# Optimization experiments

Measured on AMD Instinct MI355X. Metric: run time of the kernel, lower is better.

Reference implementation:

```python
import jax, jax.numpy as jnp
import numpy as np

UNITS = 512
LN_EPS = 1e-3  # Keras LayerNormalization default epsilon


def _lstm_cell(x, h, c, W, U, b):
    # Keras LSTMCell: z = x@W + h@U + b, gate order [i, f, g, o]
    z = x @ W + h @ U + b
    i, f, g, o = jnp.split(z, 4, axis=-1)
    i = jax.nn.sigmoid(i)
    f = jax.nn.sigmoid(f)
    g = jnp.tanh(g)
    o = jax.nn.sigmoid(o)
    c_new = f * c + i * g
    h_new = o * jnp.tanh(c_new)
    return h_new, c_new


def _layernorm(x, gamma, beta):
    mu = jnp.mean(x, axis=-1, keepdims=True)
    var = jnp.mean(jnp.square(x - mu), axis=-1, keepdims=True)
    return (x - mu) * jax.lax.rsqrt(var + LN_EPS) * gamma + beta


def setup_inputs() -> dict:
    key = jax.random.key(0)
    ks = jax.random.split(key, 8)
    B, T, F, U, C = 128, 1000, 72, UNITS, 14
    s = 0.05
    return {
        "x": jax.random.normal(ks[0], (B, T, F), jnp.float32),
        "w0": jax.random.normal(ks[1], (F, 4 * U), jnp.float32) * s,
        "u0": jax.random.normal(ks[2], (U, 4 * U), jnp.float32) * s,
        "b0": jnp.zeros((4 * U,), jnp.float32),
        "gamma": jnp.ones((U,), jnp.float32),
        "beta": jnp.zeros((U,), jnp.float32),
        "w1": jax.random.normal(ks[3], (U, 4 * U), jnp.float32) * s,
        "u1": jax.random.normal(ks[4], (U, 4 * U), jnp.float32) * s,
        "b1": jnp.zeros((4 * U,), jnp.float32),
        "wf": jax.random.normal(ks[5], (U, C), jnp.float32) * s,
        "bf": jnp.zeros((C,), jnp.float32),
    }


def reference(x, w0, u0, b0, gamma, beta, w1, u1, b1, wf, bf):
    B = x.shape[0]
    U = UNITS
    xt = jnp.transpose(x, (1, 0, 2))  # [T, B, F] time-major
    init = (
        jnp.zeros((B, U), x.dtype), jnp.zeros((B, U), x.dtype),  # h0, c0
        jnp.zeros((B, U), x.dtype), jnp.zeros((B, U), x.dtype),  # h1, c1
    )

    def step(carry, x_t):
        h0, c0, h1, c1 = carry
        h0, c0 = _lstm_cell(x_t, h0, c0, w0, u0, b0)
        h0n = _layernorm(h0, gamma, beta)
        h1, c1 = _lstm_cell(h0n, h1, c1, w1, u1, b1)
        # dropout is identity at inference (training=False)
        y_t = jax.nn.softmax(h1 @ wf + bf, axis=-1)
        return (h0, c0, h1, c1), y_t

    _, ys = jax.lax.scan(step, init, xt)  # ys: [T, B, C]
    return jnp.transpose(ys, (1, 0, 2))   # [B, T, C]
```

## Files before the change

### kernel.cpp

```cpp
#include <hip/hip_runtime.h>
#include <cstdint>
#include <cstddef>

#define T_STEPS 1000
#define NU      512
#define NC      14
#define K0TOT   592
#define K1TOT   1024

#define OFF_BP0   0
#define SZ_BP0    (128*K0TOT*16)
#define OFF_BP1   (OFF_BP0 + SZ_BP0)
#define SZ_BP1    (128*K1TOT*16)
#define OFF_S1P   (OFF_BP1 + SZ_BP1)
#define OFF_ZB1P  (OFF_S1P + 2048)
#define OFF_B0P   (OFF_ZB1P + 2048)
#define OFF_H0T   (OFF_B0P + 2048)
#define OFF_H1T   (OFF_H0T + 2*65536)
#define OFF_H1N   (OFF_H1T + 2*65536)
#define OFF_WFT   (OFF_H1N + 2*65536)
#define OFF_BAR   (OFF_WFT + 14*512)

__global__ void pack0_kernel(const float* __restrict__ w0, const float* __restrict__ u0,
                             float* __restrict__ bp0)
{
    int blk = blockIdx.x;
    int ntile = blk / 10, kc = blk % 10;
    int k0 = kc * 64;
#pragma unroll
    for (int p = 0; p < 4; p++) {
        int e = threadIdx.x + p * 256;
        int kr = e >> 4, c = e & 15;
        int k = k0 + kr;
        if (k < K0TOT) {
            int u = c >> 2, g = c & 3;
            int zcol = ntile * 4 + u + 512 * g;
            float v;
            if (k < 72)        v = w0[k * 2048 + zcol];
            else if (k < 80)   v = 0.f;
            else               v = u0[(k - 80) * 2048 + zcol];
            bp0[((size_t)ntile * K0TOT + k) * 16 + c] = v;
        }
    }
}

__global__ void pack1_kernel(const float* __restrict__ w1, const float* __restrict__ u1,
                             const float* __restrict__ gamma, float* __restrict__ bp1)
{
    int blk = blockIdx.x;
    int ntile = blk >> 4, kc = blk & 15;
    int k0 = kc * 64;
#pragma unroll
    for (int p = 0; p < 4; p++) {
        int e = threadIdx.x + p * 256;
        int kr = e >> 4, c = e & 15;
        int k = k0 + kr;
        int u = c >> 2, g = c & 3;
        int zcol = ntile * 4 + u + 512 * g;
        float v = (k < NU) ? gamma[k] * w1[k * 2048 + zcol]
                           : u1[(k - NU) * 2048 + zcol];
        bp1[((size_t)ntile * K1TOT + k) * 16 + c] = v;
    }
}

__global__ void sums_kernel(const float* __restrict__ w1, const float* __restrict__ gamma,
                            const float* __restrict__ beta, const float* __restrict__ b0,
                            const float* __restrict__ b1,
                            float* __restrict__ s1p, float* __restrict__ zb1p,
                            float* __restrict__ b0p)
{
    int zcol = blockIdx.x * 256 + threadIdx.x;
    float gs = 0.f, bs = 0.f;
    for (int k = 0; k < NU; k++) {
        float w = w1[k * 2048 + zcol];
        gs += gamma[k] * w;
        bs += beta[k] * w;
    }
    int g = zcol >> 9, r = zcol & 511, nt = r >> 2, u = r & 3;
    int pc = nt * 16 + u * 4 + g;
    s1p[pc]  = gs;
    zb1p[pc] = b1[zcol] + bs;
    b0p[pc]  = b0[zcol];
}

__global__ void wft_kernel(const float* __restrict__ wf, float* __restrict__ wfT)
{
    int i = blockIdx.x * 512 + threadIdx.x;
    if (i < NC * NU) {
        int c = i >> 9, u = i & 511;
        wfT[c * NU + u] = wf[u * NC + c];
    }
}

__global__ void init_kernel(float* __restrict__ ws)
{
    size_t i = (size_t)blockIdx.x * 1024 + threadIdx.x;
    if (i < (size_t)6 * 65536) ws[OFF_H0T + i] = 0.f;
    if (i == 0) *((unsigned*)(ws + OFF_BAR)) = 0u;
}

__device__ __forceinline__ float sigf(float x)     { return 1.f / (1.f + __expf(-x)); }
__device__ __forceinline__ float tanhfast(float x) { return 2.f / (1.f + __expf(-2.f * x)) - 1.f; }

__device__ __forceinline__ void fma8(float acc[8], float a, float4 b0, float4 b1)
{
    acc[0] = fmaf(a, b0.x, acc[0]); acc[1] = fmaf(a, b0.y, acc[1]);
    acc[2] = fmaf(a, b0.z, acc[2]); acc[3] = fmaf(a, b0.w, acc[3]);
    acc[4] = fmaf(a, b1.x, acc[4]); acc[5] = fmaf(a, b1.y, acc[5]);
    acc[6] = fmaf(a, b1.z, acc[6]); acc[7] = fmaf(a, b1.w, acc[7]);
}

__device__ __forceinline__ void reduce_zex(float acc[4][8], float* __restrict__ zex,
                                           int kw, int ch, int rg, int ks)
{
#pragma unroll
    for (int r = 0; r < 4; ++r)
#pragma unroll
        for (int c = 0; c < 8; ++c) {
            float v = acc[r][c];
            v += __shfl_xor(v, 16);
            v += __shfl_xor(v, 32);
            acc[r][c] = v;
        }
    const int zb = kw * 1088 + ch * 8;
#pragma unroll
    for (int r = 0; r < 4; ++r) {
        if (ks == r) {
#pragma unroll
            for (int c = 0; c < 8; ++c)
                zex[zb + (rg * 4 + r) * 17 + c] = acc[r][c];
        }
    }
}

__device__ __forceinline__ void grid_barrier(unsigned* bar)
{
    __syncthreads();
    if (threadIdx.x == 0) {
        __threadfence();
        unsigned old = __hip_atomic_fetch_add(bar, 1u, __ATOMIC_RELAXED, __HIP_MEMORY_SCOPE_AGENT);
        unsigned target = (old | 255u) + 1u;
        while (__hip_atomic_load(bar, __ATOMIC_RELAXED, __HIP_MEMORY_SCOPE_AGENT) < target)
            __builtin_amdgcn_s_sleep(2);
        __threadfence();
    }
    __syncthreads();
}

__device__ void ypass(const float* __restrict__ h1r, const float* __restrict__ wfT,
                      const float* __restrict__ bf, float* __restrict__ out,
                      int b, int tw, int lane)
{
    const float* hr = h1r + (size_t)b * NU + lane * 8;
    float4 hA = *(const float4*)hr;
    float4 hB = *(const float4*)(hr + 4);
    float z[NC];
#pragma unroll
    for (int c = 0; c < NC; ++c) {
        const float* wp = wfT + c * NU + lane * 8;
        float4 wA = *(const float4*)wp;
        float4 wB = *(const float4*)(wp + 4);
        float a = hA.x * wA.x;
        a = fmaf(hA.y, wA.y, a); a = fmaf(hA.z, wA.z, a); a = fmaf(hA.w, wA.w, a);
        a = fmaf(hB.x, wB.x, a); a = fmaf(hB.y, wB.y, a);
        a = fmaf(hB.z, wB.z, a); a = fmaf(hB.w, wB.w, a);
        z[c] = a;
    }
#pragma unroll
    for (int off = 32; off > 0; off >>= 1) {
#pragma unroll
        for (int c = 0; c < NC; ++c) z[c] += __shfl_xor(z[c], off);
    }
    if (lane == 0) {
        float m = -1e30f;
#pragma unroll
        for (int c = 0; c < NC; ++c) { z[c] += bf[c]; m = fmaxf(m, z[c]); }
        float s = 0.f, e[NC];
#pragma unroll
        for (int c = 0; c < NC; ++c) { e[c] = __expf(z[c] - m); s += e[c]; }
        float inv = 1.f / s;
        float* o = out + ((size_t)b * T_STEPS + tw) * NC;
#pragma unroll
        for (int c = 0; c < NC; ++c) o[c] = e[c] * inv;
    }
}

__global__ __launch_bounds__(512, 2)
void lstm_main(const float* __restrict__ x,
               const float* __restrict__ bf,
               float* __restrict__ ws, float* __restrict__ out)
{
    __shared__ float bpA_lds[K0TOT * 16];
    __shared__ float bpB_lds[K1TOT * 16];
    __shared__ float xs[64 * 81];
    __shared__ float zex[4 * 64 * 17];
    __shared__ float sq[64 * 17];

    const float* __restrict__ bp0g = ws + OFF_BP0;
    const float* __restrict__ bp1g = ws + OFF_BP1;
    const float* __restrict__ s1p  = ws + OFF_S1P;
    const float* __restrict__ zb1p = ws + OFF_ZB1P;
    const float* __restrict__ b0p  = ws + OFF_B0P;
    float* __restrict__ h0T = ws + OFF_H0T;
    float* __restrict__ h1T = ws + OFF_H1T;
    float* __restrict__ h1n = ws + OFF_H1N;
    const float* __restrict__ wfT = ws + OFF_WFT;
    unsigned* bar = (unsigned*)(ws + OFF_BAR);

    const int tid  = threadIdx.x;
    const int lane = tid & 63;
    const int w    = tid >> 6;
    const int kw   = w >> 1;
    const int ch   = w & 1;
    const int rg   = lane & 15;
    const int ks   = lane >> 4;
    const int rg4  = rg * 4;
    const int blk = blockIdx.x;
    const int mtile = blk & 1, ntile = blk >> 1;
    const int rb = mtile * 64;

    {
        const float* s0 = bp0g + (size_t)ntile * (K0TOT * 16);
        for (int i = tid; i < K0TOT * 16; i += 512) bpA_lds[i] = s0[i];
        const float* s1 = bp1g + (size_t)ntile * (K1TOT * 16);
        for (int i = tid; i < K1TOT * 16; i += 512) bpB_lds[i] = s1[i];
        for (int i = tid; i < 64 * 81; i += 512) xs[i] = 0.f;
    }
    __syncthreads();

    const int eb = tid & 63, eu = (tid >> 6) & 3;
    float c0v = 0.f, c1v = 0.f;
    float4 b0v = {0,0,0,0}, s1v = {0,0,0,0}, zbv = {0,0,0,0};
    if (tid < 256) {
        b0v = *(const float4*)&b0p[ntile * 16 + eu * 4];
        s1v = *(const float4*)&s1p[ntile * 16 + eu * 4];
        zbv = *(const float4*)&zb1p[ntile * 16 + eu * 4];
    }
    const float* xrowbase = x + (size_t)rb * 72000;

#pragma unroll 1
    for (int t = 0; t < T_STEPS; ++t) {
        const float* __restrict__ h0prev  = h0T + ((t + 1) & 1) * 65536;
        float* __restrict__       h0cur   = h0T + (t & 1) * 65536;
        const float* __restrict__ h1prev  = h1T + ((t + 1) & 1) * 65536;
        float* __restrict__       h1cur   = h1T + (t & 1) * 65536;
        const float* __restrict__ h1nprev = h1n + ((t + 1) & 1) * 65536;
        float* __restrict__       h1ncur  = h1n + (t & 1) * 65536;

        float xr[9];
#pragma unroll
        for (int j = 0; j < 9; ++j) {
            int e = tid + j * 512, row = e / 72, f = e - row * 72;
            xr[j] = xrowbase[(size_t)row * 72000 + t * 72 + f];
        }
#pragma unroll
        for (int j = 0; j < 9; ++j) {
            int e = tid + j * 512, row = e / 72, f = e - row * 72;
            xs[row * 81 + f] = xr[j];
        }
        __syncthreads();

        {
            float acc[4][8];
#pragma unroll
            for (int r = 0; r < 4; ++r)
#pragma unroll
                for (int c = 0; c < 8; ++c) acc[r][c] = 0.f;

            if (kw == 0) {
#pragma unroll 4
                for (int i = 0; i < 20; ++i) {
                    const int k = 4 * i + ks;
                    const float* bp = &bpA_lds[k * 16 + ch * 8];
                    const float4 bA = *(const float4*)bp;
                    const float4 bB = *(const float4*)(bp + 4);
                    fma8(acc[0], xs[(rg4 + 0) * 81 + k], bA, bB);
                    fma8(acc[1], xs[(rg4 + 1) * 81 + k], bA, bB);
                    fma8(acc[2], xs[(rg4 + 2) * 81 + k], bA, bB);
                    fma8(acc[3], xs[(rg4 + 3) * 81 + k], bA, bB);
                }
#pragma unroll 4
                for (int i = 20; i < 37; ++i) {
                    const int k = 4 * i + ks;
                    const float4 av = *(const float4*)(h0prev + (size_t)(k - 80) * 128 + rb + rg4);
                    const float* bp = &bpA_lds[k * 16 + ch * 8];
                    const float4 bA = *(const float4*)bp;
                    const float4 bB = *(const float4*)(bp + 4);
                    fma8(acc[0], av.x, bA, bB); fma8(acc[1], av.y, bA, bB);
                    fma8(acc[2], av.z, bA, bB); fma8(acc[3], av.w, bA, bB);
                }
            } else {
                const int kbase = kw * 148;
#pragma unroll 4
                for (int i = 0; i < 37; ++i) {
                    const int k = kbase + 4 * i + ks;
                    const float4 av = *(const float4*)(h0prev + (size_t)(k - 80) * 128 + rb + rg4);
                    const float* bp = &bpA_lds[k * 16 + ch * 8];
                    const float4 bA = *(const float4*)bp;
                    const float4 bB = *(const float4*)(bp + 4);
                    fma8(acc[0], av.x, bA, bB); fma8(acc[1], av.y, bA, bB);
                    fma8(acc[2], av.z, bA, bB); fma8(acc[3], av.w, bA, bB);
                }
            }
            reduce_zex(acc, zex, kw, ch, rg, ks);
        }
        __syncthreads();
        if (tid < 256) {
            float z[4];
#pragma unroll
            for (int g = 0; g < 4; ++g) {
                int ci = eb * 17 + eu * 4 + g;
                z[g] = zex[ci] + zex[1088 + ci] + zex[2176 + ci] + zex[3264 + ci];
            }
            z[0] += b0v.x; z[1] += b0v.y; z[2] += b0v.z; z[3] += b0v.w;
            float ig = sigf(z[0]), fg = sigf(z[1]), gg = tanhfast(z[2]), og = sigf(z[3]);
            float cn = fg * c0v + ig * gg;
            c0v = cn;
            h0cur[(ntile * 4 + eu) * 128 + rb + eb] = og * tanhfast(cn);
        }

        grid_barrier(bar);

        {
            float s = 0.f, q = 0.f;
            const float* hp = h0cur + (size_t)(w * 64) * 128 + rb + lane;
#pragma unroll 8
            for (int kk = 0; kk < 64; ++kk) {
                float v = hp[(size_t)kk * 128];
                s += v; q = fmaf(v, v, q);
            }
            sq[lane * 17 + w * 2]     = s;
            sq[lane * 17 + w * 2 + 1] = q;
        }

        if (blk < 128 && w == 0 && t > 0) ypass(h1nprev, wfT, bf, out, blk, t - 1, lane);

        {
            float acc[4][8];
#pragma unroll
            for (int r = 0; r < 4; ++r)
#pragma unroll
                for (int c = 0; c < 8; ++c) acc[r][c] = 0.f;

            const float* __restrict__ Asrc = (kw < 2) ? h0cur : h1prev;
            const int kofs   = (kw & 1) * 256;
            const int kb_lds = kw * 256;
#pragma unroll 4
            for (int i = 0; i < 64; ++i) {
                const int kk = 4 * i + ks;
                const float4 av = *(const float4*)(Asrc + (size_t)(kofs + kk) * 128 + rb + rg4);
                const float* bp = &bpB_lds[(kb_lds + kk) * 16 + ch * 8];
                const float4 bA = *(const float4*)bp;
                const float4 bB = *(const float4*)(bp + 4);
                fma8(acc[0], av.x, bA, bB); fma8(acc[1], av.y, bA, bB);
                fma8(acc[2], av.z, bA, bB); fma8(acc[3], av.w, bA, bB);
            }
            reduce_zex(acc, zex, kw, ch, rg, ks);
        }
        __syncthreads();
        if (tid < 256) {
            float s = 0.f, q = 0.f;
#pragma unroll
            for (int w8 = 0; w8 < 8; ++w8) {
                s += sq[eb * 17 + w8 * 2];
                q += sq[eb * 17 + w8 * 2 + 1];
            }
            float m  = s * (1.f / 512.f);
            float rs = rsqrtf(q * (1.f / 512.f) - m * m + 1e-3f);
            float z[4];
#pragma unroll
            for (int g = 0; g < 4; ++g) {
                int ci = eb * 17 + eu * 4 + g;
                float zG = zex[ci] + zex[1088 + ci];
                float zU = zex[2176 + ci] + zex[3264 + ci];
                float s1g = (g == 0) ? s1v.x : (g == 1) ? s1v.y : (g == 2) ? s1v.z : s1v.w;
                float zbg = (g == 0) ? zbv.x : (g == 1) ? zbv.y : (g == 2) ? zbv.z : zbv.w;
                z[g] = rs * (zG - m * s1g) + zU + zbg;
            }
            float ig = sigf(z[0]), fg = sigf(z[1]), gg = tanhfast(z[2]), og = sigf(z[3]);
            float cn = fg * c1v + ig * gg;
            c1v = cn;
            float hv = og * tanhfast(cn);
            h1cur[(ntile * 4 + eu) * 128 + rb + eb] = hv;
            h1ncur[(size_t)(rb + eb) * 512 + ntile * 4 + eu] = hv;
        }
    }

    grid_barrier(bar);
    if (blk < 128 && w == 0)
        ypass(h1n + ((T_STEPS - 1) & 1) * 65536, wfT, bf, out, blk, T_STEPS - 1, lane);
}

extern "C" void kernel_launch(void* const* d_in, const int* in_sizes, int n_in,
                              void* d_out, int out_size, void* d_ws, size_t ws_size,
                              hipStream_t stream)
{
    const float* x     = (const float*)d_in[0];
    const float* w0    = (const float*)d_in[1];
    const float* u0    = (const float*)d_in[2];
    const float* b0    = (const float*)d_in[3];
    const float* gamma = (const float*)d_in[4];
    const float* beta  = (const float*)d_in[5];
    const float* w1    = (const float*)d_in[6];
    const float* u1    = (const float*)d_in[7];
    const float* b1    = (const float*)d_in[8];
    const float* wf    = (const float*)d_in[9];
    const float* bf    = (const float*)d_in[10];
    float* out = (float*)d_out;
    float* ws  = (float*)d_ws;

    hipLaunchKernelGGL(pack0_kernel, dim3(128 * 10), dim3(256), 0, stream, w0, u0, ws + OFF_BP0);
    hipLaunchKernelGGL(pack1_kernel, dim3(128 * 16), dim3(256), 0, stream, w1, u1, gamma, ws + OFF_BP1);
    hipLaunchKernelGGL(sums_kernel, dim3(8), dim3(256), 0, stream,
                       w1, gamma, beta, b0, b1, ws + OFF_S1P, ws + OFF_ZB1P, ws + OFF_B0P);
    hipLaunchKernelGGL(wft_kernel, dim3(14), dim3(512), 0, stream, wf, ws + OFF_WFT);
    hipLaunchKernelGGL(init_kernel, dim3(384), dim3(1024), 0, stream, ws);

    const float* xp  = x;
    const float* bfp = bf;
    float* wsp  = ws;
    float* outp = out;
    void* args[] = { (void*)&xp, (void*)&bfp, (void*)&wsp, (void*)&outp };
    hipLaunchCooperativeKernel((void*)lstm_main, dim3(256), dim3(512), args, 0, stream);
}
```

Measured before the change: 34.31 ms.

## Replace FP32 FMA GEMMs with split-bf16 MFMA (hi/lo, three products)

Replaces the scalar FP32 FMA matmuls in both LSTM layers with bf16 MFMA 16x16x32 instructions. Each operand is split into a high and a low bf16 part, and three MFMA products (hh, lh, hl) are summed to get close to FP32 accuracy. Weights are pre-packed into MFMA fragment layout, hidden states are stored row-major as hi/lo bf16 pairs, and the layer-norm statistics are now computed from the A fragments inside the GEMM loop. This cuts per-step VALU work in the latency-bound recurrent loop, at the cost of extra conversion work and a small precision loss from dropping the lo*lo term.

After: 44.54 ms. 29.8% more time.

```diff
diff --git a/kernel.cpp b/kernel.cpp
--- a/kernel.cpp
+++ b/kernel.cpp
@@ -3,63 +3,85 @@
 #include <cstddef>
 
 #define T_STEPS 1000
-#define NU      512
-#define NC      14
-#define K0TOT   592
-#define K1TOT   1024
-
-#define OFF_BP0   0
-#define SZ_BP0    (128*K0TOT*16)
-#define OFF_BP1   (OFF_BP0 + SZ_BP0)
-#define SZ_BP1    (128*K1TOT*16)
-#define OFF_S1P   (OFF_BP1 + SZ_BP1)
-#define OFF_ZB1P  (OFF_S1P + 2048)
-#define OFF_B0P   (OFF_ZB1P + 2048)
-#define OFF_H0T   (OFF_B0P + 2048)
-#define OFF_H1T   (OFF_H0T + 2*65536)
-#define OFF_H1N   (OFF_H1T + 2*65536)
-#define OFF_WFT   (OFF_H1N + 2*65536)
-#define OFF_BAR   (OFF_WFT + 14*512)
+#define NU 512
+#define NC 14
+
+typedef unsigned short ushort_t;
+typedef unsigned int uint_t;
+typedef __attribute__((ext_vector_type(8))) short bf16x8;
+typedef __attribute__((ext_vector_type(4))) float f32x4;
+
+#define OFF_BP0H  0u
+#define OFF_BP0L  (OFF_BP0H + 128u*9728u*2u)
+#define OFF_BP1H  (OFF_BP0L + 128u*9728u*2u)
+#define OFF_BP1L  (OFF_BP1H + 128u*16384u*2u)
+#define OFF_S1P   (OFF_BP1L + 128u*16384u*2u)
+#define OFF_ZB1P  (OFF_S1P  + 2048u*4u)
+#define OFF_B0P   (OFF_ZB1P + 2048u*4u)
+#define OFF_WFT   (OFF_B0P  + 2048u*4u)
+#define OFF_H0H   (OFF_WFT  + 14u*512u*4u)
+#define OFF_H0L   (OFF_H0H  + 2u*128u*512u*2u)
+#define OFF_H1H   (OFF_H0L  + 2u*128u*512u*2u)
+#define OFF_H1L   (OFF_H1H  + 2u*128u*512u*2u)
+#define OFF_BAR   (OFF_H1L  + 2u*128u*512u*2u)
+
+__device__ __host__ __forceinline__ float bf2f(short s) {
+    unsigned u = ((unsigned)(unsigned short)s) << 16;
+    return __builtin_bit_cast(float, u);
+}
+__device__ __forceinline__ ushort_t f2bf(float f) {
+    unsigned u = __float_as_uint(f);
+    u = u + 0x7FFFu + ((u >> 16) & 1u);
+    return (ushort_t)(u >> 16);
+}
 
 __global__ void pack0_kernel(const float* __restrict__ w0, const float* __restrict__ u0,
-                             float* __restrict__ bp0)
-{
-    int blk = blockIdx.x;
-    int ntile = blk / 10, kc = blk % 10;
-    int k0 = kc * 64;
-#pragma unroll
-    for (int p = 0; p < 4; p++) {
-        int e = threadIdx.x + p * 256;
-        int kr = e >> 4, c = e & 15;
-        int k = k0 + kr;
-        if (k < K0TOT) {
-            int u = c >> 2, g = c & 3;
-            int zcol = ntile * 4 + u + 512 * g;
+                             ushort_t* __restrict__ bp0h, ushort_t* __restrict__ bp0l)
+{
+    const int ntile = blockIdx.x;
+    const int l = threadIdx.x & 63;
+    const int c = l & 15, koff = (l >> 4) * 8;
+    const int zcol = ntile * 4 + (c >> 2) + 512 * (c & 3);
+    for (int s = (threadIdx.x >> 6); s < 19; s += 4) {
+        bf16x8 hv, lv;
+#pragma unroll
+        for (int j = 0; j < 8; ++j) {
+            int k = s * 32 + koff + j;
             float v;
-            if (k < 72)        v = w0[k * 2048 + zcol];
-            else if (k < 80)   v = 0.f;
-            else               v = u0[(k - 80) * 2048 + zcol];
-            bp0[((size_t)ntile * K0TOT + k) * 16 + c] = v;
-        }
+            if (k < 96) v = (k < 72) ? w0[(size_t)k * 2048 + zcol] : 0.f;
+            else        v = u0[(size_t)(k - 96) * 2048 + zcol];
+            ushort_t hi = f2bf(v);
+            ushort_t lo = f2bf(v - bf2f((short)hi));
+            hv[j] = (short)hi; lv[j] = (short)lo;
+        }
+        size_t di = ((size_t)(ntile * 19 + s) * 64 + l) * 8;
+        *(bf16x8*)&bp0h[di] = hv;
+        *(bf16x8*)&bp0l[di] = lv;
     }
 }
 
 __global__ void pack1_kernel(const float* __restrict__ w1, const float* __restrict__ u1,
-                             const float* __restrict__ gamma, float* __restrict__ bp1)
-{
-    int blk = blockIdx.x;
-    int ntile = blk >> 4, kc = blk & 15;
-    int k0 = kc * 64;
-#pragma unroll
-    for (int p = 0; p < 4; p++) {
-        int e = threadIdx.x + p * 256;
-        int kr = e >> 4, c = e & 15;
-        int k = k0 + kr;
-        int u = c >> 2, g = c & 3;
-        int zcol = ntile * 4 + u + 512 * g;
-        float v = (k < NU) ? gamma[k] * w1[k * 2048 + zcol]
-                           : u1[(k - NU) * 2048 + zcol];
-        bp1[((size_t)ntile * K1TOT + k) * 16 + c] = v;
+                             const float* __restrict__ gamma,
+                             ushort_t* __restrict__ bp1h, ushort_t* __restrict__ bp1l)
+{
+    const int ntile = blockIdx.x;
+    const int l = threadIdx.x & 63;
+    const int c = l & 15, koff = (l >> 4) * 8;
+    const int zcol = ntile * 4 + (c >> 2) + 512 * (c & 3);
+    for (int s = (threadIdx.x >> 6); s < 32; s += 4) {
+        bf16x8 hv, lv;
+#pragma unroll
+        for (int j = 0; j < 8; ++j) {
+            int k = s * 32 + koff + j;
+            float v = (k < 512) ? gamma[k] * w1[(size_t)k * 2048 + zcol]
+                                : u1[(size_t)(k - 512) * 2048 + zcol];
+            ushort_t hi = f2bf(v);
+            ushort_t lo = f2bf(v - bf2f((short)hi));
+            hv[j] = (short)hi; lv[j] = (short)lo;
+        }
+        size_t di = ((size_t)(ntile * 32 + s) * 64 + l) * 8;
+        *(bf16x8*)&bp1h[di] = hv;
+        *(bf16x8*)&bp1l[di] = lv;
     }
 }
 
@@ -72,7 +94,7 @@
     int zcol = blockIdx.x * 256 + threadIdx.x;
     float gs = 0.f, bs = 0.f;
     for (int k = 0; k < NU; k++) {
-        float w = w1[k * 2048 + zcol];
+        float w = w1[(size_t)k * 2048 + zcol];
         gs += gamma[k] * w;
         bs += beta[k] * w;
     }
@@ -88,50 +110,20 @@
     int i = blockIdx.x * 512 + threadIdx.x;
     if (i < NC * NU) {
         int c = i >> 9, u = i & 511;
-        wfT[c * NU + u] = wf[u * NC + c];
-    }
-}
-
-__global__ void init_kernel(float* __restrict__ ws)
+        wfT[c * NU + u] = wf[(size_t)u * NC + c];
+    }
+}
+
+__global__ void init_kernel(char* __restrict__ ws)
 {
     size_t i = (size_t)blockIdx.x * 1024 + threadIdx.x;
-    if (i < (size_t)6 * 65536) ws[OFF_H0T + i] = 0.f;
-    if (i == 0) *((unsigned*)(ws + OFF_BAR)) = 0u;
+    uint_t* st = (uint_t*)(ws + OFF_H0H);
+    if (i < 262144) st[i] = 0u;
+    if (i == 0) *(unsigned*)(ws + OFF_BAR) = 0u;
 }
 
 __device__ __forceinline__ float sigf(float x)     { return 1.f / (1.f + __expf(-x)); }
 __device__ __forceinline__ float tanhfast(float x) { return 2.f / (1.f + __expf(-2.f * x)) - 1.f; }
-
-__device__ __forceinline__ void fma8(float acc[8], float a, float4 b0, float4 b1)
-{
-    acc[0] = fmaf(a, b0.x, acc[0]); acc[1] = fmaf(a, b0.y, acc[1]);
-    acc[2] = fmaf(a, b0.z, acc[2]); acc[3] = fmaf(a, b0.w, acc[3]);
-    acc[4] = fmaf(a, b1.x, acc[4]); acc[5] = fmaf(a, b1.y, acc[5]);
-    acc[6] = fmaf(a, b1.z, acc[6]); acc[7] = fmaf(a, b1.w, acc[7]);
-}
-
-__device__ __forceinline__ void reduce_zex(float acc[4][8], float* __restrict__ zex,
-                                           int kw, int ch, int rg, int ks)
-{
-#pragma unroll
-    for (int r = 0; r < 4; ++r)
-#pragma unroll
-        for (int c = 0; c < 8; ++c) {
-            float v = acc[r][c];
-            v += __shfl_xor(v, 16);
-            v += __shfl_xor(v, 32);
-            acc[r][c] = v;
-        }
-    const int zb = kw * 1088 + ch * 8;
-#pragma unroll
-    for (int r = 0; r < 4; ++r) {
-        if (ks == r) {
-#pragma unroll
-            for (int c = 0; c < 8; ++c)
-                zex[zb + (rg * 4 + r) * 17 + c] = acc[r][c];
-        }
-    }
-}
 
 __device__ __forceinline__ void grid_barrier(unsigned* bar)
 {
@@ -147,23 +139,22 @@
     __syncthreads();
 }
 
-__device__ void ypass(const float* __restrict__ h1r, const float* __restrict__ wfT,
-                      const float* __restrict__ bf, float* __restrict__ out,
-                      int b, int tw, int lane)
-{
-    const float* hr = h1r + (size_t)b * NU + lane * 8;
-    float4 hA = *(const float4*)hr;
-    float4 hB = *(const float4*)(hr + 4);
+__device__ void ypass(const ushort_t* __restrict__ h1h, const ushort_t* __restrict__ h1l,
+                      const float* __restrict__ wfT, const float* __restrict__ bf,
+                      float* __restrict__ out, int b, int tw, int lane)
+{
+    bf16x8 hh = *(const bf16x8*)(h1h + (size_t)b * NU + lane * 8);
+    bf16x8 hl = *(const bf16x8*)(h1l + (size_t)b * NU + lane * 8);
+    float hv[8];
+#pragma unroll
+    for (int j = 0; j < 8; ++j) hv[j] = bf2f(hh[j]) + bf2f(hl[j]);
     float z[NC];
 #pragma unroll
     for (int c = 0; c < NC; ++c) {
         const float* wp = wfT + c * NU + lane * 8;
-        float4 wA = *(const float4*)wp;
-        float4 wB = *(const float4*)(wp + 4);
-        float a = hA.x * wA.x;
-        a = fmaf(hA.y, wA.y, a); a = fmaf(hA.z, wA.z, a); a = fmaf(hA.w, wA.w, a);
-        a = fmaf(hB.x, wB.x, a); a = fmaf(hB.y, wB.y, a);
-        a = fmaf(hB.z, wB.z, a); a = fmaf(hB.w, wB.w, a);
+        float a = 0.f;
+#pragma unroll
+        for (int j = 0; j < 8; ++j) a = fmaf(hv[j], wp[j], a);
         z[c] = a;
     }
 #pragma unroll
@@ -185,210 +176,212 @@
     }
 }
 
-__global__ __launch_bounds__(512, 2)
-void lstm_main(const float* __restrict__ x,
-               const float* __restrict__ bf,
-               float* __restrict__ ws, float* __restrict__ out)
-{
-    __shared__ float bpA_lds[K0TOT * 16];
-    __shared__ float bpB_lds[K1TOT * 16];
-    __shared__ float xs[64 * 81];
-    __shared__ float zex[4 * 64 * 17];
-    __shared__ float sq[64 * 17];
-
-    const float* __restrict__ bp0g = ws + OFF_BP0;
-    const float* __restrict__ bp1g = ws + OFF_BP1;
-    const float* __restrict__ s1p  = ws + OFF_S1P;
-    const float* __restrict__ zb1p = ws + OFF_ZB1P;
-    const float* __restrict__ b0p  = ws + OFF_B0P;
-    float* __restrict__ h0T = ws + OFF_H0T;
-    float* __restrict__ h1T = ws + OFF_H1T;
-    float* __restrict__ h1n = ws + OFF_H1N;
-    const float* __restrict__ wfT = ws + OFF_WFT;
+#define MFMA(A,B,C) __builtin_amdgcn_mfma_f32_16x16x32_bf16((A),(B),(C),0,0,0)
+
+__global__ __launch_bounds__(512, 1)
+void lstm_main(const float* __restrict__ x, const float* __restrict__ bf,
+               char* __restrict__ ws, float* __restrict__ out)
+{
+    __shared__ __attribute__((aligned(16))) ushort_t bpAh[19*512];
+    __shared__ __attribute__((aligned(16))) ushort_t bpAl[19*512];
+    __shared__ __attribute__((aligned(16))) ushort_t bpBh[32*512];
+    __shared__ __attribute__((aligned(16))) ushort_t bpBl[32*512];
+    __shared__ __attribute__((aligned(16))) ushort_t xsh[12*512];
+    __shared__ __attribute__((aligned(16))) ushort_t xsl[12*512];
+    __shared__ float zexf[2*64*17];
+    __shared__ float sqs[64], sqq[64];
+
+    const ushort_t* __restrict__ bp0h = (const ushort_t*)(ws + OFF_BP0H);
+    const ushort_t* __restrict__ bp0l = (const ushort_t*)(ws + OFF_BP0L);
+    const ushort_t* __restrict__ bp1h = (const ushort_t*)(ws + OFF_BP1H);
+    const ushort_t* __restrict__ bp1l = (const ushort_t*)(ws + OFF_BP1L);
+    const float* __restrict__ s1p  = (const float*)(ws + OFF_S1P);
+    const float* __restrict__ zb1p = (const float*)(ws + OFF_ZB1P);
+    const float* __restrict__ b0p  = (const float*)(ws + OFF_B0P);
+    const float* __restrict__ wfT  = (const float*)(ws + OFF_WFT);
+    ushort_t* h0h = (ushort_t*)(ws + OFF_H0H);
+    ushort_t* h0l = (ushort_t*)(ws + OFF_H0L);
+    ushort_t* h1h = (ushort_t*)(ws + OFF_H1H);
+    ushort_t* h1l = (ushort_t*)(ws + OFF_H1L);
     unsigned* bar = (unsigned*)(ws + OFF_BAR);
 
-    const int tid  = threadIdx.x;
-    const int lane = tid & 63;
-    const int w    = tid >> 6;
-    const int kw   = w >> 1;
-    const int ch   = w & 1;
-    const int rg   = lane & 15;
-    const int ks   = lane >> 4;
-    const int rg4  = rg * 4;
-    const int blk = blockIdx.x;
-    const int mtile = blk & 1, ntile = blk >> 1;
+    const int tid = threadIdx.x;
+    const int l   = tid & 63;
+    const int w   = tid >> 6;
+    const int m   = w & 3;
+    const int kw  = w >> 2;
+    const int rr  = l & 15;
+    const int koff = (l >> 4) * 8;
+    const int blk = blockIdx.x, mtile = blk & 1, ntile = blk >> 1;
     const int rb = mtile * 64;
+    const int rowA = rb + m * 16 + rr;
 
     {
-        const float* s0 = bp0g + (size_t)ntile * (K0TOT * 16);
-        for (int i = tid; i < K0TOT * 16; i += 512) bpA_lds[i] = s0[i];
-        const float* s1 = bp1g + (size_t)ntile * (K1TOT * 16);
-        for (int i = tid; i < K1TOT * 16; i += 512) bpB_lds[i] = s1[i];
-        for (int i = tid; i < 64 * 81; i += 512) xs[i] = 0.f;
-    }
-    __syncthreads();
+        const uint_t* s0h = (const uint_t*)bp0h + (size_t)ntile * 4864;
+        const uint_t* s0l = (const uint_t*)bp0l + (size_t)ntile * 4864;
+        uint_t* d0h = (uint_t*)bpAh; uint_t* d0l = (uint_t*)bpAl;
+        for (int i = tid; i < 4864; i += 512) { d0h[i] = s0h[i]; d0l[i] = s0l[i]; }
+        const uint_t* s1h = (const uint_t*)bp1h + (size_t)ntile * 8192;
+        const uint_t* s1l = (const uint_t*)bp1l + (size_t)ntile * 8192;
+        uint_t* d1h = (uint_t*)bpBh; uint_t* d1l = (uint_t*)bpBl;
+        for (int i = tid; i < 8192; i += 512) { d1h[i] = s1h[i]; d1l[i] = s1l[i]; }
+    }
 
     const int eb = tid & 63, eu = (tid >> 6) & 3;
     float c0v = 0.f, c1v = 0.f;
-    float4 b0v = {0,0,0,0}, s1v = {0,0,0,0}, zbv = {0,0,0,0};
+    f32x4 b0v = {0,0,0,0}, s1v = {0,0,0,0}, zbv = {0,0,0,0};
     if (tid < 256) {
-        b0v = *(const float4*)&b0p[ntile * 16 + eu * 4];
-        s1v = *(const float4*)&s1p[ntile * 16 + eu * 4];
-        zbv = *(const float4*)&zb1p[ntile * 16 + eu * 4];
-    }
-    const float* xrowbase = x + (size_t)rb * 72000;
+        b0v = *(const f32x4*)&b0p[ntile * 16 + eu * 4];
+        s1v = *(const f32x4*)&s1p[ntile * 16 + eu * 4];
+        zbv = *(const f32x4*)&zb1p[ntile * 16 + eu * 4];
+    }
+    __syncthreads();
 
 #pragma unroll 1
     for (int t = 0; t < T_STEPS; ++t) {
-        const float* __restrict__ h0prev  = h0T + ((t + 1) & 1) * 65536;
-        float* __restrict__       h0cur   = h0T + (t & 1) * 65536;
-        const float* __restrict__ h1prev  = h1T + ((t + 1) & 1) * 65536;
-        float* __restrict__       h1cur   = h1T + (t & 1) * 65536;
-        const float* __restrict__ h1nprev = h1n + ((t + 1) & 1) * 65536;
-        float* __restrict__       h1ncur  = h1n + (t & 1) * 65536;
-
-        float xr[9];
-#pragma unroll
-        for (int j = 0; j < 9; ++j) {
-            int e = tid + j * 512, row = e / 72, f = e - row * 72;
-            xr[j] = xrowbase[(size_t)row * 72000 + t * 72 + f];
-        }
-#pragma unroll
-        for (int j = 0; j < 9; ++j) {
-            int e = tid + j * 512, row = e / 72, f = e - row * 72;
-            xs[row * 81 + f] = xr[j];
-        }
+        const int cur = t & 1, prv = cur ^ 1;
+        ushort_t* __restrict__       h0h_cur = h0h + cur * 65536;
+        ushort_t* __restrict__       h0l_cur = h0l + cur * 65536;
+        const ushort_t* __restrict__ h0h_prv = h0h + prv * 65536;
+        const ushort_t* __restrict__ h0l_prv = h0l + prv * 65536;
+        ushort_t* __restrict__       h1h_cur = h1h + cur * 65536;
+        ushort_t* __restrict__       h1l_cur = h1l + cur * 65536;
+        const ushort_t* __restrict__ h1h_prv = h1h + prv * 65536;
+        const ushort_t* __restrict__ h1l_prv = h1l + prv * 65536;
+
+        for (int i = tid; i < 3072; i += 512) { ((uint_t*)xsh)[i] = 0u; ((uint_t*)xsl)[i] = 0u; }
         __syncthreads();
+#pragma unroll
+        for (int i = 0; i < 9; ++i) {
+            int e = tid + i * 512;
+            int row = e / 72, k = e - row * 72;
+            float v = x[(size_t)(rb + row) * 72000 + (size_t)t * 72 + k];
+            ushort_t hi = f2bf(v);
+            ushort_t lo = f2bf(v - bf2f((short)hi));
+            int di = (((row >> 4) * 3 + (k >> 5)) * 64 + ((k >> 3) & 3) * 16 + (row & 15)) * 8 + (k & 7);
+            xsh[di] = hi; xsl[di] = lo;
+        }
+        __syncthreads();
 
         {
-            float acc[4][8];
-#pragma unroll
-            for (int r = 0; r < 4; ++r)
-#pragma unroll
-                for (int c = 0; c < 8; ++c) acc[r][c] = 0.f;
-
+            f32x4 aHH = {0,0,0,0}, aLH = {0,0,0,0}, aHL = {0,0,0,0};
             if (kw == 0) {
-#pragma unroll 4
-                for (int i = 0; i < 20; ++i) {
-                    const int k = 4 * i + ks;
-                    const float* bp = &bpA_lds[k * 16 + ch * 8];
-                    const float4 bA = *(const float4*)bp;
-                    const float4 bB = *(const float4*)(bp + 4);
-                    fma8(acc[0], xs[(rg4 + 0) * 81 + k], bA, bB);
-                    fma8(acc[1], xs[(rg4 + 1) * 81 + k], bA, bB);
-                    fma8(acc[2], xs[(rg4 + 2) * 81 + k], bA, bB);
-                    fma8(acc[3], xs[(rg4 + 3) * 81 + k], bA, bB);
+#pragma unroll
+                for (int s = 0; s < 3; ++s) {
+                    bf16x8 ah = *(const bf16x8*)&xsh[((m * 3 + s) * 64 + l) * 8];
+                    bf16x8 al = *(const bf16x8*)&xsl[((m * 3 + s) * 64 + l) * 8];
+                    bf16x8 bh = *(const bf16x8*)&bpAh[s * 512 + l * 8];
+                    bf16x8 bl = *(const bf16x8*)&bpAl[s * 512 + l * 8];
+                    aHH = MFMA(ah, bh, aHH); aLH = MFMA(al, bh, aLH); aHL = MFMA(ah, bl, aHL);
                 }
-#pragma unroll 4
-                for (int i = 20; i < 37; ++i) {
-                    const int k = 4 * i + ks;
-                    const float4 av = *(const float4*)(h0prev + (size_t)(k - 80) * 128 + rb + rg4);
-                    const float* bp = &bpA_lds[k * 16 + ch * 8];
-                    const float4 bA = *(const float4*)bp;
-                    const float4 bB = *(const float4*)(bp + 4);
-                    fma8(acc[0], av.x, bA, bB); fma8(acc[1], av.y, bA, bB);
-                    fma8(acc[2], av.z, bA, bB); fma8(acc[3], av.w, bA, bB);
+#pragma unroll
+                for (int s = 3; s < 10; ++s) {
+                    const int ko = (s - 3) * 32 + koff;
+                    bf16x8 ah = *(const bf16x8*)(h0h_prv + rowA * 512 + ko);
+                    bf16x8 al = *(const bf16x8*)(h0l_prv + rowA * 512 + ko);
+                    bf16x8 bh = *(const bf16x8*)&bpAh[s * 512 + l * 8];
+                    bf16x8 bl = *(const bf16x8*)&bpAl[s * 512 + l * 8];
+                    aHH = MFMA(ah, bh, aHH); aLH = MFMA(al, bh, aLH); aHL = MFMA(ah, bl, aHL);
                 }
             } else {
-                const int kbase = kw * 148;
-#pragma unroll 4
-                for (int i = 0; i < 37; ++i) {
-                    const int k = kbase + 4 * i + ks;
-                    const float4 av = *(const float4*)(h0prev + (size_t)(k - 80) * 128 + rb + rg4);
-                    const float* bp = &bpA_lds[k * 16 + ch * 8];
-                    const float4 bA = *(const float4*)bp;
-                    const float4 bB = *(const float4*)(bp + 4);
-                    fma8(acc[0], av.x, bA, bB); fma8(acc[1], av.y, bA, bB);
-                    fma8(acc[2], av.z, bA, bB); fma8(acc[3], av.w, bA, bB);
+#pragma unroll
+                for (int s = 10; s < 19; ++s) {
+                    const int ko = (s - 3) * 32 + koff;
+                    bf16x8 ah = *(const bf16x8*)(h0h_prv + rowA * 512 + ko);
+                    bf16x8 al = *(const bf16x8*)(h0l_prv + rowA * 512 + ko);
+                    bf16x8 bh = *(const bf16x8*)&bpAh[s * 512 + l * 8];
+                    bf16x8 bl = *(const bf16x8*)&bpAl[s * 512 + l * 8];
+                    aHH = MFMA(ah, bh, aHH); aLH = MFMA(al, bh, aLH); aHL = MFMA(ah, bl, aHL);
                 }
             }
-            reduce_zex(acc, zex, kw, ch, rg, ks);
+            f32x4 zv = aHH + aLH + aHL;
+#pragma unroll
+            for (int r = 0; r < 4; ++r)
+                zexf[kw * 1088 + (m * 16 + (l >> 4) * 4 + r) * 17 + rr] = zv[r];
         }
         __syncthreads();
         if (tid < 256) {
             float z[4];
 #pragma unroll
-            for (int g = 0; g < 4; ++g) {
-                int ci = eb * 17 + eu * 4 + g;
-                z[g] = zex[ci] + zex[1088 + ci] + zex[2176 + ci] + zex[3264 + ci];
-            }
+            for (int g = 0; g < 4; ++g)
+                z[g] = zexf[eb * 17 + eu * 4 + g] + zexf[1088 + eb * 17 + eu * 4 + g];
             z[0] += b0v.x; z[1] += b0v.y; z[2] += b0v.z; z[3] += b0v.w;
             float ig = sigf(z[0]), fg = sigf(z[1]), gg = tanhfast(z[2]), og = sigf(z[3]);
             float cn = fg * c0v + ig * gg;
             c0v = cn;
-            h0cur[(ntile * 4 + eu) * 128 + rb + eb] = og * tanhfast(cn);
+            float hval = og * tanhfast(cn);
+            ushort_t hi = f2bf(hval);
+            ushort_t lo = f2bf(hval - bf2f((short)hi));
+            int hidx = (rb + eb) * 512 + ntile * 4 + eu;
+            h0h_cur[hidx] = hi; h0l_cur[hidx] = lo;
         }
 
         grid_barrier(bar);
 
         {
-            float s = 0.f, q = 0.f;
-            const float* hp = h0cur + (size_t)(w * 64) * 128 + rb + lane;
-#pragma unroll 8
-            for (int kk = 0; kk < 64; ++kk) {
-                float v = hp[(size_t)kk * 128];
-                s += v; q = fmaf(v, v, q);
+            f32x4 bHH = {0,0,0,0}, bLH = {0,0,0,0}, bHL = {0,0,0,0};
+            const ushort_t* __restrict__ Ah = kw ? h1h_prv : h0h_cur;
+            const ushort_t* __restrict__ Al = kw ? h1l_prv : h0l_cur;
+            float sa = 0.f, qa = 0.f;
+#pragma unroll
+            for (int s2 = 0; s2 < 16; ++s2) {
+                const int ko = s2 * 32 + koff;
+                bf16x8 ah = *(const bf16x8*)(Ah + rowA * 512 + ko);
+                bf16x8 al = *(const bf16x8*)(Al + rowA * 512 + ko);
+                const int sb = (kw * 16 + s2) * 512 + l * 8;
+                bf16x8 bh = *(const bf16x8*)&bpBh[sb];
+                bf16x8 bl = *(const bf16x8*)&bpBl[sb];
+                bHH = MFMA(ah, bh, bHH); bLH = MFMA(al, bh, bLH); bHL = MFMA(ah, bl, bHL);
+                if (kw == 0) {
+#pragma unroll
+                    for (int j = 0; j < 8; ++j) {
+                        float hv = bf2f(ah[j]) + bf2f(al[j]);
+                        sa += hv; qa = fmaf(hv, hv, qa);
+                    }
+                }
             }
-            sq[lane * 17 + w * 2]     = s;
-            sq[lane * 17 + w * 2 + 1] = q;
-        }
-
-        if (blk < 128 && w == 0 && t > 0) ypass(h1nprev, wfT, bf, out, blk, t - 1, lane);
-
-        {
-            float acc[4][8];
+            if (kw == 0) {
+                sa += __shfl_xor(sa, 16); sa += __shfl_xor(sa, 32);
+                qa += __shfl_xor(qa, 16); qa += __shfl_xor(qa, 32);
+                if (l < 16) { sqs[m * 16 + l] = sa; sqq[m * 16 + l] = qa; }
+            }
+            f32x4 zv = bHH + bLH + bHL;
 #pragma unroll
             for (int r = 0; r < 4; ++r)
-#pragma unroll
-                for (int c = 0; c < 8; ++c) acc[r][c] = 0.f;
-
-            const float* __restrict__ Asrc = (kw < 2) ? h0cur : h1prev;
-            const int kofs   = (kw & 1) * 256;
-            const int kb_lds = kw * 256;
-#pragma unroll 4
-            for (int i = 0; i < 64; ++i) {
-                const int kk = 4 * i + ks;
-                const float4 av = *(const float4*)(Asrc + (size_t)(kofs + kk) * 128 + rb + rg4);
-                const float* bp = &bpB_lds[(kb_lds + kk) * 16 + ch * 8];
-                const float4 bA = *(const float4*)bp;
-                const float4 bB = *(const float4*)(bp + 4);
-                fma8(acc[0], av.x, bA, bB); fma8(acc[1], av.y, bA, bB);
-                fma8(acc[2], av.z, bA, bB); fma8(acc[3], av.w, bA, bB);
-            }
-            reduce_zex(acc, zex, kw, ch, rg, ks);
+                zexf[kw * 1088 + (m * 16 + (l >> 4) * 4 + r) * 17 + rr] = zv[r];
         }
         __syncthreads();
+
+        if (blk < 128 && w == 7 && t > 0)
+            ypass(h1h_prv, h1l_prv, wfT, bf, out, blk, t - 1, l);
+
         if (tid < 256) {
-            float s = 0.f, q = 0.f;
-#pragma unroll
-            for (int w8 = 0; w8 < 8; ++w8) {
-                s += sq[eb * 17 + w8 * 2];
-                q += sq[eb * 17 + w8 * 2 + 1];
-            }
-            float m  = s * (1.f / 512.f);
-            float rs = rsqrtf(q * (1.f / 512.f) - m * m + 1e-3f);
+            float mu = sqs[eb] * (1.f / 512.f);
+            float rs = rsqrtf(sqq[eb] * (1.f / 512.f) - mu * mu + 1e-3f);
             float z[4];
 #pragma unroll
             for (int g = 0; g < 4; ++g) {
-                int ci = eb * 17 + eu * 4 + g;
-                float zG = zex[ci] + zex[1088 + ci];
-                float zU = zex[2176 + ci] + zex[3264 + ci];
+                float zG = zexf[eb * 17 + eu * 4 + g];
+                float zU = zexf[1088 + eb * 17 + eu * 4 + g];
                 float s1g = (g == 0) ? s1v.x : (g == 1) ? s1v.y : (g == 2) ? s1v.z : s1v.w;
                 float zbg = (g == 0) ? zbv.x : (g == 1) ? zbv.y : (g == 2) ? zbv.z : zbv.w;
-                z[g] = rs * (zG - m * s1g) + zU + zbg;
+                z[g] = rs * (zG - mu * s1g) + zU + zbg;
             }
             float ig = sigf(z[0]), fg = sigf(z[1]), gg = tanhfast(z[2]), og = sigf(z[3]);
             float cn = fg * c1v + ig * gg;
             c1v = cn;
-            float hv = og * tanhfast(cn);
-            h1cur[(ntile * 4 + eu) * 128 + rb + eb] = hv;
-            h1ncur[(size_t)(rb + eb) * 512 + ntile * 4 + eu] = hv;
+            float hval = og * tanhfast(cn);
+            ushort_t hi = f2bf(hval);
+            ushort_t lo = f2bf(hval - bf2f((short)hi));
+            int hidx = (rb + eb) * 512 + ntile * 4 + eu;
+            h1h_cur[hidx] = hi; h1l_cur[hidx] = lo;
         }
     }
 
     grid_barrier(bar);
-    if (blk < 128 && w == 0)
-        ypass(h1n + ((T_STEPS - 1) & 1) * 65536, wfT, bf, out, blk, T_STEPS - 1, lane);
+    if (blk < 128 && w == 7)
+        ypass(h1h + ((T_STEPS - 1) & 1) * 65536, h1l + ((T_STEPS - 1) & 1) * 65536,
+              wfT, bf, out, blk, T_STEPS - 1, l);
 }
 
 extern "C" void kernel_launch(void* const* d_in, const int* in_sizes, int n_in,
@@ -407,18 +400,21 @@
     const float* wf    = (const float*)d_in[9];
     const float* bf    = (const float*)d_in[10];
     float* out = (float*)d_out;
-    float* ws  = (float*)d_ws;
-
-    hipLaunchKernelGGL(pack0_kernel, dim3(128 * 10), dim3(256), 0, stream, w0, u0, ws + OFF_BP0);
-    hipLaunchKernelGGL(pack1_kernel, dim3(128 * 16), dim3(256), 0, stream, w1, u1, gamma, ws + OFF_BP1);
+    char* ws   = (char*)d_ws;
+
+    hipLaunchKernelGGL(pack0_kernel, dim3(128), dim3(256), 0, stream,
+                       w0, u0, (ushort_t*)(ws + OFF_BP0H), (ushort_t*)(ws + OFF_BP0L));
+    hipLaunchKernelGGL(pack1_kernel, dim3(128), dim3(256), 0, stream,
+                       w1, u1, gamma, (ushort_t*)(ws + OFF_BP1H), (ushort_t*)(ws + OFF_BP1L));
     hipLaunchKernelGGL(sums_kernel, dim3(8), dim3(256), 0, stream,
-                       w1, gamma, beta, b0, b1, ws + OFF_S1P, ws + OFF_ZB1P, ws + OFF_B0P);
-    hipLaunchKernelGGL(wft_kernel, dim3(14), dim3(512), 0, stream, wf, ws + OFF_WFT);
-    hipLaunchKernelGGL(init_kernel, dim3(384), dim3(1024), 0, stream, ws);
+                       w1, gamma, beta, b0, b1,
+                       (float*)(ws + OFF_S1P), (float*)(ws + OFF_ZB1P), (float*)(ws + OFF_B0P));
+    hipLaunchKernelGGL(wft_kernel, dim3(14), dim3(512), 0, stream, wf, (float*)(ws + OFF_WFT));
+    hipLaunchKernelGGL(init_kernel, dim3(256), dim3(1024), 0, stream, ws);
 
     const float* xp  = x;
     const float* bfp = bf;
-    float* wsp  = ws;
+    char*  wsp  = ws;
     float* outp = out;
     void* args[] = { (void*)&xp, (void*)&bfp, (void*)&wsp, (void*)&outp };
     hipLaunchCooperativeKernel((void*)lstm_main, dim3(256), dim3(512), args, 0, stream);
```
